# Performance work log

Measured on AMD Instinct MI355X. Metric: run time of the kernel, lower is better.

The kernel has to match this reference:

```python
import jax, jax.numpy as jnp
import numpy as np

CUTOFF = 6.0   # matches init cutoff
D = 32         # descriptor/MLP width
NTYPES = 3     # len(type_map)


def setup_inputs() -> dict:
    key = jax.random.key(0)
    ks = jax.random.split(key, 13)
    b, n, m, n_ghost = 2, 8192, 64, 512
    neighbor_vectors = jax.random.normal(ks[0], (b, n, m, 4), jnp.float32)
    element_map = jax.random.randint(ks[1], (b, n), 0, NTYPES, jnp.int32)
    central_atoms = jax.random.randint(ks[2], (b, n), 0, n, jnp.int32)
    neighbor_indices = jax.random.randint(ks[3], (b, n, m), 0, n + n_ghost, jnp.int32)
    neighbor_types = jax.random.randint(ks[4], (b, n, m), 0, NTYPES, jnp.int32)
    type_embed = 0.1 * jax.random.normal(ks[5], (NTYPES, D), jnp.float32)
    elem_bias = 0.1 * jax.random.normal(ks[6], (NTYPES,), jnp.float32)
    W1 = 0.5 * jax.random.normal(ks[7], (4, D), jnp.float32)
    b1 = 0.1 * jax.random.normal(ks[8], (D,), jnp.float32)
    W2 = (1.0 / np.sqrt(D)) * jax.random.normal(ks[9], (D, D), jnp.float32)
    b2 = 0.1 * jax.random.normal(ks[10], (D,), jnp.float32)
    W3 = (1.0 / np.sqrt(D)) * jax.random.normal(ks[11], (D, 1), jnp.float32)
    b3 = 0.1 * jax.random.normal(ks[12], (1,), jnp.float32)
    return dict(element_map=element_map, central_atoms=central_atoms,
                neighbor_indices=neighbor_indices, neighbor_types=neighbor_types,
                neighbor_vectors=neighbor_vectors, n_ghost=n_ghost,
                type_embed=type_embed, elem_bias=elem_bias,
                W1=W1, b1=b1, W2=W2, b2=b2, W3=W3, b3=b3)


def _field_Ei(rel, element_map, neighbor_types, type_embed, elem_bias, W1, b1, W2, b2, W3, b3):
    # rel: [b,n,m,3] relative positions; recompute distance as the torch forward does
    dist = jnp.linalg.norm(rel, axis=-1, keepdims=True)                 # [b,n,m,1]
    fc = 0.5 * (jnp.cos(jnp.pi * jnp.minimum(dist, CUTOFF) / CUTOFF) + 1.0)
    s = jnp.exp(-dist) * fc                                             # smooth radial weight
    feat = jnp.concatenate([s, s * rel], axis=-1)                       # [b,n,m,4]
    h = jnp.tanh(feat @ W1 + b1 + type_embed[neighbor_types])           # [b,n,m,D]
    g = h.mean(axis=2)                                                  # pool over neighbors -> [b,n,D]
    h2 = jnp.tanh(g @ W2 + b2)                                          # [b,n,D]
    Ei = h2 @ W3 + b3 + elem_bias[element_map][..., None]               # [b,n,1]
    return Ei


def derive_mechanics(grad_Ei, neighbor_vectors, neighbor_indices, n_ghost):
    # grad_Ei: [b,n,m,3] = d(sum Ei)/d r_ij, with r_ij = r_j - r_i
    b, n, m, _ = grad_Ei.shape
    ntot = n + n_ghost
    bidx = jnp.arange(b)[:, None, None]
    # force on central atom i: +sum_j dE/dr_ij ; reaction scattered to neighbor j: -dE/dr_ij
    force = jnp.zeros((b, ntot, 3), grad_Ei.dtype)
    force = force.at[:, :n].add(grad_Ei.sum(axis=2))
    force = force.at[bidx, neighbor_indices].add(-grad_Ei)
    rij = neighbor_vectors[..., 1:]                                     # [b,n,m,3]
    pv = (rij[..., :, None] * grad_Ei[..., None, :]).reshape(b, n, m, 9)  # pair virial r (x) dE
    virial = pv.sum(axis=(1, 2))                                        # [b,9]
    av = jnp.zeros((b, ntot, 9), grad_Ei.dtype)
    av = av.at[bidx, neighbor_indices].add(pv)
    return force[:, :n], virial, av[:, :n]


def reference(element_map, central_atoms, neighbor_indices, neighbor_types,
              neighbor_vectors, n_ghost, type_embed, elem_bias,
              W1, b1, W2, b2, W3, b3):
    rel = neighbor_vectors[..., 1:]                                     # [b,n,m,3]

    def ei_sum(r):
        Ei = _field_Ei(r, element_map, neighbor_types, type_embed, elem_bias,
                       W1, b1, W2, b2, W3, b3)
        return Ei.sum(), Ei

    grad_Ei, Ei = jax.grad(ei_sum, has_aux=True)(rel)                   # matches autograd.grad w/ ones mask
    Etot = Ei.sum(axis=1)                                               # [b,1]
    dist = jnp.linalg.norm(rel, axis=-1, keepdims=True)
    nv = jnp.concatenate([dist, rel], axis=-1)
    force, virial, atomic_virial = derive_mechanics(grad_Ei, nv, neighbor_indices, n_ghost)
    return Etot, Ei, force, virial, atomic_virial
```

## Files before the change

kernel.cpp:

```cpp
#include <hip/hip_runtime.h>

#define CUTOFF_F 6.0f
#define PI_F 3.14159265358979323846f
#define CAP 112

typedef __fp16 fp16x2 __attribute__((ext_vector_type(2)));

__device__ __forceinline__ unsigned pk2(float a, float b) {
  union { fp16x2 h; unsigned u; } cv;
  cv.h = __builtin_amdgcn_cvt_pkrtz(a, b);
  return cv.u;
}
__device__ __forceinline__ float f16bits(unsigned v) {
  union { unsigned short u; __fp16 h; } cv; cv.u = (unsigned short)v; return (float)cv.h;
}

template<int CTRL>
__device__ __forceinline__ float dpp_add(float x) {
  int y = __builtin_amdgcn_update_dpp(0, __float_as_int(x), CTRL, 0xf, 0xf, true);
  return x + __int_as_float(y);
}
__device__ __forceinline__ float wave_sum63(float x) {
  x = dpp_add<0x111>(x);
  x = dpp_add<0x112>(x);
  x = dpp_add<0x114>(x);
  x = dpp_add<0x118>(x);
  x = dpp_add<0x142>(x);
  x = dpp_add<0x143>(x);
  return x;
}

__device__ __forceinline__ float fast_tanh(float x) {
  float e = __expf(2.0f * x);
  return 1.0f - 2.0f * __builtin_amdgcn_rcpf(e + 1.0f);
}

__global__ __launch_bounds__(256) void field_main(
    const int* __restrict__ element_map,
    const int* __restrict__ neighbor_indices,
    const int* __restrict__ neighbor_types,
    const float4* __restrict__ neighbor_vectors,
    const float* __restrict__ type_embed,
    const float* __restrict__ elem_bias,
    const float* __restrict__ W1,
    const float* __restrict__ b1,
    const float* __restrict__ W2,
    const float* __restrict__ b2,
    const float* __restrict__ W3,
    const float* __restrict__ b3,
    float* __restrict__ outEi,
    int* __restrict__ counts,
    float* __restrict__ obuf,
    float4* __restrict__ bucket,
    float* __restrict__ partials,
    int n)
{
  __shared__ float4 sW1t[32];
  __shared__ float  sbte[3][32];
  __shared__ float  sW2[32 * 33];
  __shared__ float  sW3[32];
  __shared__ float  sb2[32];
  __shared__ float  sElemBias[3];
  __shared__ float  sb3;
  __shared__ float  blkEi[4];
  __shared__ float  blkVir[4][9];
  __shared__ unsigned hbuf[4][64][17];
  __shared__ float    gtd[4][3][32];

  const int tid = threadIdx.x;

  if (tid < 32) {
    sW1t[tid] = make_float4(W1[tid], W1[32 + tid], W1[64 + tid], W1[96 + tid]);
    sW3[tid]  = W3[tid];
    sb2[tid]  = b2[tid];
  } else if (tid < 128) {
    int t = (tid - 32) >> 5, k = tid & 31;
    sbte[t][k] = b1[k] + type_embed[t * 32 + k];
  } else if (tid == 128) {
    sb3 = b3[0];
  } else if (tid < 132) {
    sElemBias[tid - 129] = elem_bias[tid - 129];
  }
  for (int i = tid; i < 1024; i += 256) {
    int l = i >> 5, k = i & 31;
    sW2[l * 33 + k] = W2[i];
  }
  __syncthreads();

  const int wave = tid >> 6;
  const int lane = tid & 63;
  const int atom = blockIdx.x * 4 + wave;
  const int bb = atom / n;

  const int base = atom * 64 + lane;
  const int idx = neighbor_indices[base];
  const int dest = bb * n + idx;
  const int em = element_map[atom];

  int pos = 0;
  const bool real = (idx < n);
  if (real) pos = atomicAdd(&counts[dest], 1);

  const float4 nv = neighbor_vectors[base];
  const float rx = nv.y, ry = nv.z, rz = nv.w;
  const int typ = neighbor_types[base];

  const float d2 = rx * rx + ry * ry + rz * rz;
  const float d = sqrtf(d2);
  const float invd = (d > 0.0f) ? __builtin_amdgcn_rcpf(d) : 0.0f;
  float s, sp;
  if (d < CUTOFF_F) {
    const float arg = d * (PI_F / CUTOFF_F);
    const float cs = __cosf(arg);
    const float sn = __sinf(arg);
    const float e = __expf(-d);
    const float fc = 0.5f * (cs + 1.0f);
    const float fcp = -(0.5f * PI_F / CUTOFF_F) * sn;
    s = e * fc;
    sp = e * (fcp - fc);
  } else {
    s = 0.0f;
    sp = 0.0f;
  }
  const float f1 = s * rx, f2 = s * ry, f3 = s * rz;

  float h[32];
#pragma unroll
  for (int k = 0; k < 32; k += 2) {
    const float4 wa = sW1t[k];
    float pa = sbte[typ][k];
    pa = fmaf(s, wa.x, pa); pa = fmaf(f1, wa.y, pa);
    pa = fmaf(f2, wa.z, pa); pa = fmaf(f3, wa.w, pa);
    h[k] = fast_tanh(pa);
    const float4 wb = sW1t[k + 1];
    float pb = sbte[typ][k + 1];
    pb = fmaf(s, wb.x, pb); pb = fmaf(f1, wb.y, pb);
    pb = fmaf(f2, wb.z, pb); pb = fmaf(f3, wb.w, pb);
    h[k + 1] = fast_tanh(pb);
    hbuf[wave][lane][k >> 1] = pk2(h[k], h[k + 1]);
  }

  const int halfid = lane >> 5;
  const int kd = lane & 31;
  const int dw = kd >> 1;
  const int sh = (kd & 1) << 4;
  float gsum = 0.0f;
#pragma unroll
  for (int j = 0; j < 32; ++j) {
    const unsigned w = hbuf[wave][j + (halfid << 5)][dw];
    gsum += f16bits(w >> sh);
  }
  gsum += __shfl_xor(gsum, 32);
  const float gk = gsum * (1.0f / 64.0f);
  if (halfid == 0) gtd[wave][0][kd] = gk;

  float acc = sb2[kd];
#pragma unroll
  for (int l = 0; l < 32; l += 4) {
    const float4 g4 = *(const float4*)&gtd[wave][0][l];
    acc = fmaf(g4.x, sW2[(l + 0) * 33 + kd], acc);
    acc = fmaf(g4.y, sW2[(l + 1) * 33 + kd], acc);
    acc = fmaf(g4.z, sW2[(l + 2) * 33 + kd], acc);
    acc = fmaf(g4.w, sW2[(l + 3) * 33 + kd], acc);
  }
  const float h2 = fast_tanh(acc);
  const float tl = (1.0f - h2 * h2) * sW3[kd];
  if (halfid == 0) gtd[wave][1][kd] = tl;

  float dgacc = 0.0f;
#pragma unroll
  for (int l = 0; l < 32; l += 4) {
    const float4 t4 = *(const float4*)&gtd[wave][1][l];
    dgacc = fmaf(t4.x, sW2[kd * 33 + l + 0], dgacc);
    dgacc = fmaf(t4.y, sW2[kd * 33 + l + 1], dgacc);
    dgacc = fmaf(t4.z, sW2[kd * 33 + l + 2], dgacc);
    dgacc = fmaf(t4.w, sW2[kd * 33 + l + 3], dgacc);
  }
  if (halfid == 0) gtd[wave][2][kd] = dgacc * (1.0f / 64.0f);

  float p = h2 * sW3[kd];

  float q0 = 0.0f, q1 = 0.0f, q2 = 0.0f, q3 = 0.0f;
#pragma unroll
  for (int k = 0; k < 32; k += 4) {
    const float4 d4 = *(const float4*)&gtd[wave][2][k];
#pragma unroll
    for (int u = 0; u < 4; ++u) {
      const float dgk = (u == 0) ? d4.x : (u == 1) ? d4.y : (u == 2) ? d4.z : d4.w;
      const float hk = h[k + u];
      const float dpre = dgk * (1.0f - hk * hk);
      const float4 w = sW1t[k + u];
      q0 = fmaf(dpre, w.x, q0);
      q1 = fmaf(dpre, w.y, q1);
      q2 = fmaf(dpre, w.z, q2);
      q3 = fmaf(dpre, w.w, q3);
    }
  }

  const float common = sp * invd * (q0 + q1 * rx + q2 * ry + q3 * rz);
  const float gx = fmaf(common, rx, s * q1);
  const float gy = fmaf(common, ry, s * q2);
  const float gz = fmaf(common, rz, s * q3);

  if (real) {
    if (pos < CAP) {
      float4 pay;
      pay.x = __uint_as_float(pk2(gx, gy));
      pay.y = __uint_as_float(pk2(gz, rx));
      pay.z = __uint_as_float(pk2(ry, rz));
      pay.w = 0.0f;
      bucket[(size_t)dest * CAP + pos] = pay;
    } else {
      float* ob = obuf + (size_t)dest * 12;
      atomicAdd(ob + 0, -gx); atomicAdd(ob + 1, -gy); atomicAdd(ob + 2, -gz);
      atomicAdd(ob + 3, rx * gx); atomicAdd(ob + 4, rx * gy); atomicAdd(ob + 5, rx * gz);
      atomicAdd(ob + 6, ry * gx); atomicAdd(ob + 7, ry * gy); atomicAdd(ob + 8, ry * gz);
      atomicAdd(ob + 9, rz * gx); atomicAdd(ob + 10, rz * gy); atomicAdd(ob + 11, rz * gz);
    }
  }

  float sfx = wave_sum63(gx);
  float sfy = wave_sum63(gy);
  float sfz = wave_sum63(gz);
  float vr0 = wave_sum63(rx * gx), vr1 = wave_sum63(rx * gy), vr2 = wave_sum63(rx * gz);
  float vr3 = wave_sum63(ry * gx), vr4 = wave_sum63(ry * gy), vr5 = wave_sum63(ry * gz);
  float vr6 = wave_sum63(rz * gx), vr7 = wave_sum63(rz * gy), vr8 = wave_sum63(rz * gz);
  float psum = wave_sum63(p) * 0.5f;

  if (lane == 63) {
    const float Ei_val = psum + sb3 + sElemBias[em];
    outEi[atom] = Ei_val;
    blkEi[wave] = Ei_val;
    blkVir[wave][0] = vr0; blkVir[wave][1] = vr1; blkVir[wave][2] = vr2;
    blkVir[wave][3] = vr3; blkVir[wave][4] = vr4; blkVir[wave][5] = vr5;
    blkVir[wave][6] = vr6; blkVir[wave][7] = vr7; blkVir[wave][8] = vr8;
    const int spos = atomicAdd(&counts[atom], 1);
    if (spos < CAP) {
      float4 pay;
      pay.x = __uint_as_float(pk2(-sfx, -sfy));
      pay.y = __uint_as_float(pk2(-sfz, 0.0f));
      pay.z = 0.0f;
      pay.w = 0.0f;
      bucket[(size_t)atom * CAP + spos] = pay;
    } else {
      float* ob = obuf + (size_t)atom * 12;
      atomicAdd(ob + 0, sfx); atomicAdd(ob + 1, sfy); atomicAdd(ob + 2, sfz);
    }
  }

  __syncthreads();
  if (tid < 9) {
    partials[blockIdx.x * 10 + tid] =
        blkVir[0][tid] + blkVir[1][tid] + blkVir[2][tid] + blkVir[3][tid];
  } else if (tid == 9) {
    partials[blockIdx.x * 10 + 9] = blkEi[0] + blkEi[1] + blkEi[2] + blkEi[3];
  }
}

__global__ __launch_bounds__(256) void field_gather(
    const int* __restrict__ counts,
    const float4* __restrict__ bucket,
    const float* __restrict__ obuf,
    float* __restrict__ outForce,
    float* __restrict__ outAV,
    int n)
{
  __shared__ float sf[4][12];
  const int tid = threadIdx.x;
  const int wave = tid >> 6;
  const int lane = tid & 63;
  const int dest = blockIdx.x * 4 + wave;

  const int rawcnt = counts[dest];
  const int cnt = (rawcnt > CAP) ? CAP : rawcnt;

  float fx = 0.0f, fy = 0.0f, fz = 0.0f;
  float a0 = 0, a1 = 0, a2 = 0, a3 = 0, a4 = 0, a5 = 0, a6 = 0, a7 = 0, a8 = 0;

#pragma unroll 2
  for (int l = lane; l < cnt; l += 64) {
    const float4 pay = bucket[(size_t)dest * CAP + l];
    const unsigned w0 = __float_as_uint(pay.x);
    const unsigned w1 = __float_as_uint(pay.y);
    const unsigned w2 = __float_as_uint(pay.z);
    const float gx = f16bits(w0), gy = f16bits(w0 >> 16);
    const float gz = f16bits(w1), rx = f16bits(w1 >> 16);
    const float ry = f16bits(w2), rz = f16bits(w2 >> 16);
    fx -= gx; fy -= gy; fz -= gz;
    a0 = fmaf(rx, gx, a0); a1 = fmaf(rx, gy, a1); a2 = fmaf(rx, gz, a2);
    a3 = fmaf(ry, gx, a3); a4 = fmaf(ry, gy, a4); a5 = fmaf(ry, gz, a5);
    a6 = fmaf(rz, gx, a6); a7 = fmaf(rz, gy, a7); a8 = fmaf(rz, gz, a8);
  }

  fx = wave_sum63(fx); fy = wave_sum63(fy); fz = wave_sum63(fz);
  a0 = wave_sum63(a0); a1 = wave_sum63(a1); a2 = wave_sum63(a2);
  a3 = wave_sum63(a3); a4 = wave_sum63(a4); a5 = wave_sum63(a5);
  a6 = wave_sum63(a6); a7 = wave_sum63(a7); a8 = wave_sum63(a8);

  if (lane == 63) {
    if (rawcnt > CAP) {
      const float* ob = obuf + (size_t)dest * 12;
      fx += ob[0]; fy += ob[1]; fz += ob[2];
      a0 += ob[3]; a1 += ob[4]; a2 += ob[5];
      a3 += ob[6]; a4 += ob[7]; a5 += ob[8];
      a6 += ob[9]; a7 += ob[10]; a8 += ob[11];
    }
    sf[wave][0] = fx; sf[wave][1] = fy; sf[wave][2] = fz;
    sf[wave][3] = a0; sf[wave][4] = a1; sf[wave][5] = a2;
    sf[wave][6] = a3; sf[wave][7] = a4; sf[wave][8] = a5;
    sf[wave][9] = a6; sf[wave][10] = a7; sf[wave][11] = a8;
  }
  __syncthreads();

  const int d0 = blockIdx.x * 4;
  if (tid < 12) {
    outForce[(size_t)d0 * 3 + tid] = sf[tid / 3][tid % 3];
  } else if (tid >= 64 && tid < 100) {
    const int t = tid - 64;
    outAV[(size_t)d0 * 9 + t] = sf[t / 9][3 + t % 9];
  }
}

__global__ __launch_bounds__(256) void field_reduce(
    const float* __restrict__ partials,
    float* __restrict__ outEtot,
    float* __restrict__ outVirial,
    int half)
{
  __shared__ float sacc[4][10];
  const int b = blockIdx.x;
  const int tid = threadIdx.x;
  const int lane = tid & 63;
  const int wave = tid >> 6;

  float acc[10] = {0, 0, 0, 0, 0, 0, 0, 0, 0, 0};
  for (int r = b * half + tid; r < (b + 1) * half; r += 256) {
#pragma unroll
    for (int t = 0; t < 10; ++t) acc[t] += partials[r * 10 + t];
  }
#pragma unroll
  for (int t = 0; t < 10; ++t) acc[t] = wave_sum63(acc[t]);
  if (lane == 63) {
#pragma unroll
    for (int t = 0; t < 10; ++t) sacc[wave][t] = acc[t];
  }
  __syncthreads();
  if (tid < 9) {
    outVirial[b * 9 + tid] = sacc[0][tid] + sacc[1][tid] + sacc[2][tid] + sacc[3][tid];
  } else if (tid == 9) {
    outEtot[b] = sacc[0][9] + sacc[1][9] + sacc[2][9] + sacc[3][9];
  }
}

extern "C" void kernel_launch(void* const* d_in, const int* in_sizes, int n_in,
                              void* d_out, int out_size, void* d_ws, size_t ws_size,
                              hipStream_t stream) {
  const int* element_map        = (const int*)d_in[0];
  const int* neighbor_indices   = (const int*)d_in[2];
  const int* neighbor_types     = (const int*)d_in[3];
  const float4* neighbor_vectors = (const float4*)d_in[4];
  const float* type_embed = (const float*)d_in[6];
  const float* elem_bias  = (const float*)d_in[7];
  const float* W1 = (const float*)d_in[8];
  const float* b1 = (const float*)d_in[9];
  const float* W2 = (const float*)d_in[10];
  const float* b2 = (const float*)d_in[11];
  const float* W3 = (const float*)d_in[12];
  const float* b3 = (const float*)d_in[13];

  const int B = 2;
  const int bn = in_sizes[0];
  const int n = bn / B;
  const int nblk = bn / 4;

  float* out = (float*)d_out;
  float* outEtot   = out;
  float* outEi     = outEtot + B;
  float* outForce  = outEi + bn;
  float* outVirial = outForce + (size_t)bn * 3;
  float* outAV     = outVirial + (size_t)B * 9;

  char* ws = (char*)d_ws;
  int* counts = (int*)ws;
  size_t countBytes = (size_t)bn * sizeof(int);
  float* obuf = (float*)(ws + countBytes);
  size_t obufBytes = (size_t)bn * 12 * sizeof(float);
  float* partials = (float*)(ws + countBytes + obufBytes);
  size_t partialBytes = (size_t)nblk * 10 * sizeof(float);
  float4* bucket = (float4*)(ws + countBytes + obufBytes + partialBytes);

  (void)hipMemsetAsync(counts, 0, countBytes + obufBytes, stream);

  dim3 grid(nblk), block(256);
  hipLaunchKernelGGL(field_main, grid, block, 0, stream,
                     element_map, neighbor_indices, neighbor_types,
                     neighbor_vectors, type_embed, elem_bias,
                     W1, b1, W2, b2, W3, b3,
                     outEi, counts, obuf, bucket, partials, n);
  hipLaunchKernelGGL(field_gather, grid, block, 0, stream,
                     counts, bucket, obuf, outForce, outAV, n);
  hipLaunchKernelGGL(field_reduce, dim3(B), block, 0, stream,
                     partials, outEtot, outVirial, nblk / B);
}
```

Before: 151.6 us.

## Split neighbor pooling into two passes, add ILP to matvecs, fuse reduce into gather

The neighbor mean-pool now runs in two 16-dimension passes over a smaller LDS staging buffer. Each pass uses all 64 lanes, 16 per dimension group, and combines them with two shuffles. The two 32x32 matvecs are split into four independent accumulator chains to shorten FMA dependency chains. The separate reduction kernel is folded into the first two blocks of the gather kernel, which removes one launch. The cost is extra shuffles and LDS round-trips in the pooling step, plus two slightly slower gather blocks.

Measured after the change: 147.8 us. 2.5% less time.

```diff
diff --git a/kernel.cpp b/kernel.cpp
--- a/kernel.cpp
+++ b/kernel.cpp
@@ -64,7 +64,7 @@
   __shared__ float  sb3;
   __shared__ float  blkEi[4];
   __shared__ float  blkVir[4][9];
-  __shared__ unsigned hbuf[4][64][17];
+  __shared__ unsigned hb[4][64][9];
   __shared__ float    gtd[4][3][32];
 
   const int tid = threadIdx.x;
@@ -125,58 +125,95 @@
   const float f1 = s * rx, f2 = s * ry, f3 = s * rz;
 
   float h[32];
-#pragma unroll
-  for (int k = 0; k < 32; k += 2) {
-    const float4 wa = sW1t[k];
-    float pa = sbte[typ][k];
-    pa = fmaf(s, wa.x, pa); pa = fmaf(f1, wa.y, pa);
-    pa = fmaf(f2, wa.z, pa); pa = fmaf(f3, wa.w, pa);
-    h[k] = fast_tanh(pa);
-    const float4 wb = sW1t[k + 1];
-    float pb = sbte[typ][k + 1];
-    pb = fmaf(s, wb.x, pb); pb = fmaf(f1, wb.y, pb);
-    pb = fmaf(f2, wb.z, pb); pb = fmaf(f3, wb.w, pb);
-    h[k + 1] = fast_tanh(pb);
-    hbuf[wave][lane][k >> 1] = pk2(h[k], h[k + 1]);
-  }
-
-  const int halfid = lane >> 5;
+  const int dim = lane & 15;
+  const int q   = lane >> 4;
+  const int w   = dim >> 1;
+  const int sh  = (dim & 1) << 4;
+
+#pragma unroll
+  for (int pass = 0; pass < 2; ++pass) {
+    const int kb = pass << 4;
+#pragma unroll
+    for (int k = 0; k < 16; k += 2) {
+      const float4 wa = sW1t[kb + k];
+      float pa = sbte[typ][kb + k];
+      pa = fmaf(s, wa.x, pa); pa = fmaf(f1, wa.y, pa);
+      pa = fmaf(f2, wa.z, pa); pa = fmaf(f3, wa.w, pa);
+      h[kb + k] = fast_tanh(pa);
+      const float4 wb = sW1t[kb + k + 1];
+      float pb = sbte[typ][kb + k + 1];
+      pb = fmaf(s, wb.x, pb); pb = fmaf(f1, wb.y, pb);
+      pb = fmaf(f2, wb.z, pb); pb = fmaf(f3, wb.w, pb);
+      h[kb + k + 1] = fast_tanh(pb);
+      hb[wave][lane][k >> 1] = pk2(h[kb + k], h[kb + k + 1]);
+    }
+    float s0 = 0.0f, s1 = 0.0f;
+#pragma unroll
+    for (int jj = 0; jj < 16; jj += 2) {
+      s0 += f16bits(hb[wave][(q << 4) + jj][w] >> sh);
+      s1 += f16bits(hb[wave][(q << 4) + jj + 1][w] >> sh);
+    }
+    float gs = s0 + s1;
+    gs += __shfl_xor(gs, 16);
+    gs += __shfl_xor(gs, 32);
+    if (lane < 16) gtd[wave][0][kb + lane] = gs * (1.0f / 64.0f);
+  }
+
   const int kd = lane & 31;
-  const int dw = kd >> 1;
-  const int sh = (kd & 1) << 4;
-  float gsum = 0.0f;
-#pragma unroll
-  for (int j = 0; j < 32; ++j) {
-    const unsigned w = hbuf[wave][j + (halfid << 5)][dw];
-    gsum += f16bits(w >> sh);
-  }
-  gsum += __shfl_xor(gsum, 32);
-  const float gk = gsum * (1.0f / 64.0f);
-  if (halfid == 0) gtd[wave][0][kd] = gk;
-
-  float acc = sb2[kd];
-#pragma unroll
-  for (int l = 0; l < 32; l += 4) {
-    const float4 g4 = *(const float4*)&gtd[wave][0][l];
-    acc = fmaf(g4.x, sW2[(l + 0) * 33 + kd], acc);
-    acc = fmaf(g4.y, sW2[(l + 1) * 33 + kd], acc);
-    acc = fmaf(g4.z, sW2[(l + 2) * 33 + kd], acc);
-    acc = fmaf(g4.w, sW2[(l + 3) * 33 + kd], acc);
-  }
+  float a0 = sb2[kd], a1 = 0.0f, a2 = 0.0f, a3 = 0.0f;
+#pragma unroll
+  for (int l = 0; l < 8; l += 4) {
+    const float4 gA = *(const float4*)&gtd[wave][0][l];
+    const float4 gB = *(const float4*)&gtd[wave][0][l + 8];
+    const float4 gC = *(const float4*)&gtd[wave][0][l + 16];
+    const float4 gD = *(const float4*)&gtd[wave][0][l + 24];
+    a0 = fmaf(gA.x, sW2[(l + 0) * 33 + kd], a0);
+    a0 = fmaf(gA.y, sW2[(l + 1) * 33 + kd], a0);
+    a0 = fmaf(gA.z, sW2[(l + 2) * 33 + kd], a0);
+    a0 = fmaf(gA.w, sW2[(l + 3) * 33 + kd], a0);
+    a1 = fmaf(gB.x, sW2[(l + 8) * 33 + kd], a1);
+    a1 = fmaf(gB.y, sW2[(l + 9) * 33 + kd], a1);
+    a1 = fmaf(gB.z, sW2[(l + 10) * 33 + kd], a1);
+    a1 = fmaf(gB.w, sW2[(l + 11) * 33 + kd], a1);
+    a2 = fmaf(gC.x, sW2[(l + 16) * 33 + kd], a2);
+    a2 = fmaf(gC.y, sW2[(l + 17) * 33 + kd], a2);
+    a2 = fmaf(gC.z, sW2[(l + 18) * 33 + kd], a2);
+    a2 = fmaf(gC.w, sW2[(l + 19) * 33 + kd], a2);
+    a3 = fmaf(gD.x, sW2[(l + 24) * 33 + kd], a3);
+    a3 = fmaf(gD.y, sW2[(l + 25) * 33 + kd], a3);
+    a3 = fmaf(gD.z, sW2[(l + 26) * 33 + kd], a3);
+    a3 = fmaf(gD.w, sW2[(l + 27) * 33 + kd], a3);
+  }
+  const float acc = (a0 + a1) + (a2 + a3);
   const float h2 = fast_tanh(acc);
   const float tl = (1.0f - h2 * h2) * sW3[kd];
-  if (halfid == 0) gtd[wave][1][kd] = tl;
-
-  float dgacc = 0.0f;
-#pragma unroll
-  for (int l = 0; l < 32; l += 4) {
-    const float4 t4 = *(const float4*)&gtd[wave][1][l];
-    dgacc = fmaf(t4.x, sW2[kd * 33 + l + 0], dgacc);
-    dgacc = fmaf(t4.y, sW2[kd * 33 + l + 1], dgacc);
-    dgacc = fmaf(t4.z, sW2[kd * 33 + l + 2], dgacc);
-    dgacc = fmaf(t4.w, sW2[kd * 33 + l + 3], dgacc);
-  }
-  if (halfid == 0) gtd[wave][2][kd] = dgacc * (1.0f / 64.0f);
+  if (lane < 32) gtd[wave][1][kd] = tl;
+
+  float b0 = 0.0f, b1v = 0.0f, b2v = 0.0f, b3v = 0.0f;
+#pragma unroll
+  for (int l = 0; l < 8; l += 4) {
+    const float4 tA = *(const float4*)&gtd[wave][1][l];
+    const float4 tB = *(const float4*)&gtd[wave][1][l + 8];
+    const float4 tC = *(const float4*)&gtd[wave][1][l + 16];
+    const float4 tD = *(const float4*)&gtd[wave][1][l + 24];
+    b0 = fmaf(tA.x, sW2[kd * 33 + l + 0], b0);
+    b0 = fmaf(tA.y, sW2[kd * 33 + l + 1], b0);
+    b0 = fmaf(tA.z, sW2[kd * 33 + l + 2], b0);
+    b0 = fmaf(tA.w, sW2[kd * 33 + l + 3], b0);
+    b1v = fmaf(tB.x, sW2[kd * 33 + l + 8], b1v);
+    b1v = fmaf(tB.y, sW2[kd * 33 + l + 9], b1v);
+    b1v = fmaf(tB.z, sW2[kd * 33 + l + 10], b1v);
+    b1v = fmaf(tB.w, sW2[kd * 33 + l + 11], b1v);
+    b2v = fmaf(tC.x, sW2[kd * 33 + l + 16], b2v);
+    b2v = fmaf(tC.y, sW2[kd * 33 + l + 17], b2v);
+    b2v = fmaf(tC.z, sW2[kd * 33 + l + 18], b2v);
+    b2v = fmaf(tC.w, sW2[kd * 33 + l + 19], b2v);
+    b3v = fmaf(tD.x, sW2[kd * 33 + l + 24], b3v);
+    b3v = fmaf(tD.y, sW2[kd * 33 + l + 25], b3v);
+    b3v = fmaf(tD.z, sW2[kd * 33 + l + 26], b3v);
+    b3v = fmaf(tD.w, sW2[kd * 33 + l + 27], b3v);
+  }
+  if (lane < 32) gtd[wave][2][kd] = ((b0 + b1v) + (b2v + b3v)) * (1.0f / 64.0f);
 
   float p = h2 * sW3[kd];
 
@@ -189,11 +226,11 @@
       const float dgk = (u == 0) ? d4.x : (u == 1) ? d4.y : (u == 2) ? d4.z : d4.w;
       const float hk = h[k + u];
       const float dpre = dgk * (1.0f - hk * hk);
-      const float4 w = sW1t[k + u];
-      q0 = fmaf(dpre, w.x, q0);
-      q1 = fmaf(dpre, w.y, q1);
-      q2 = fmaf(dpre, w.z, q2);
-      q3 = fmaf(dpre, w.w, q3);
+      const float4 wv = sW1t[k + u];
+      q0 = fmaf(dpre, wv.x, q0);
+      q1 = fmaf(dpre, wv.y, q1);
+      q2 = fmaf(dpre, wv.z, q2);
+      q3 = fmaf(dpre, wv.w, q3);
     }
   }
 
@@ -261,11 +298,15 @@
     const int* __restrict__ counts,
     const float4* __restrict__ bucket,
     const float* __restrict__ obuf,
+    const float* __restrict__ partials,
     float* __restrict__ outForce,
     float* __restrict__ outAV,
-    int n)
+    float* __restrict__ outEtot,
+    float* __restrict__ outVirial,
+    int half)
 {
   __shared__ float sf[4][12];
+  __shared__ float sacc[4][10];
   const int tid = threadIdx.x;
   const int wave = tid >> 6;
   const int lane = tid & 63;
@@ -319,36 +360,26 @@
     const int t = tid - 64;
     outAV[(size_t)d0 * 9 + t] = sf[t / 9][3 + t % 9];
   }
-}
-
-__global__ __launch_bounds__(256) void field_reduce(
-    const float* __restrict__ partials,
-    float* __restrict__ outEtot,
-    float* __restrict__ outVirial,
-    int half)
-{
-  __shared__ float sacc[4][10];
-  const int b = blockIdx.x;
-  const int tid = threadIdx.x;
-  const int lane = tid & 63;
-  const int wave = tid >> 6;
-
-  float acc[10] = {0, 0, 0, 0, 0, 0, 0, 0, 0, 0};
-  for (int r = b * half + tid; r < (b + 1) * half; r += 256) {
-#pragma unroll
-    for (int t = 0; t < 10; ++t) acc[t] += partials[r * 10 + t];
-  }
-#pragma unroll
-  for (int t = 0; t < 10; ++t) acc[t] = wave_sum63(acc[t]);
-  if (lane == 63) {
-#pragma unroll
-    for (int t = 0; t < 10; ++t) sacc[wave][t] = acc[t];
-  }
-  __syncthreads();
-  if (tid < 9) {
-    outVirial[b * 9 + tid] = sacc[0][tid] + sacc[1][tid] + sacc[2][tid] + sacc[3][tid];
-  } else if (tid == 9) {
-    outEtot[b] = sacc[0][9] + sacc[1][9] + sacc[2][9] + sacc[3][9];
+
+  if (blockIdx.x < 2) {
+    const int b = blockIdx.x;
+    float acc[10] = {0, 0, 0, 0, 0, 0, 0, 0, 0, 0};
+    for (int r = b * half + tid; r < (b + 1) * half; r += 256) {
+#pragma unroll
+      for (int t = 0; t < 10; ++t) acc[t] += partials[r * 10 + t];
+    }
+#pragma unroll
+    for (int t = 0; t < 10; ++t) acc[t] = wave_sum63(acc[t]);
+    if (lane == 63) {
+#pragma unroll
+      for (int t = 0; t < 10; ++t) sacc[wave][t] = acc[t];
+    }
+    __syncthreads();
+    if (tid < 9) {
+      outVirial[b * 9 + tid] = sacc[0][tid] + sacc[1][tid] + sacc[2][tid] + sacc[3][tid];
+    } else if (tid == 9) {
+      outEtot[b] = sacc[0][9] + sacc[1][9] + sacc[2][9] + sacc[3][9];
+    }
   }
 }
 
@@ -398,7 +429,6 @@
                      W1, b1, W2, b2, W3, b3,
                      outEi, counts, obuf, bucket, partials, n);
   hipLaunchKernelGGL(field_gather, grid, block, 0, stream,
-                     counts, bucket, obuf, outForce, outAV, n);
-  hipLaunchKernelGGL(field_reduce, dim3(B), block, 0, stream,
-                     partials, outEtot, outVirial, nblk / B);
-}
+                     counts, bucket, obuf, partials,
+                     outForce, outAV, outEtot, outVirial, nblk / B);
+}
```
